# Kernel tuning notes

Hardware: AMD Instinct MI355X
Metric: run time of the kernel (lower is better)

## Reference

```python
import jax, jax.numpy as jnp
import numpy as np

EPS = 1e-8  # matches F.cosine_similarity default eps


def setup_inputs() -> dict:
    key = jax.random.key(0)
    k1, k2 = jax.random.split(key)
    labels = jax.random.uniform(k1, (8192, 2), dtype=jnp.float32)  # argmax -> random 0/1
    datas = jax.random.normal(k2, (8192, 4096), dtype=jnp.float32)
    return {"labels": labels, "datas": datas}


def reference(labels, datas):
    # labels: [B, C] one-hot (C=2); datas: [B, D]
    lab = jnp.argmax(labels, axis=1)
    mask0 = (lab == 0).astype(datas.dtype)  # normal vectors
    mask1 = (lab == 1).astype(datas.dtype)  # except vectors
    n0 = jnp.sum(mask0)
    n1 = jnp.sum(mask1)

    # mean of label-0 rows (fixed-shape masked mean instead of boolean gather)
    mean_vec = jnp.sum(datas * mask0[:, None], axis=0) / jnp.maximum(n0, 1.0)  # [D]

    # batched cosine similarity of every row vs mean_vec (replaces per-row loop)
    x_norm = jnp.maximum(jnp.linalg.norm(datas, axis=1), EPS)  # [B]
    m_norm = jnp.maximum(jnp.linalg.norm(mean_vec), EPS)       # scalar
    cos = (datas @ mean_vec) / (x_norm * m_norm)               # [B]
    abs_cos = jnp.abs(cos)

    sim_loss = jnp.sum(mask0 * (1.0 - abs_cos)) / jnp.maximum(n0, 1.0)
    differ_loss = jnp.sum(mask1 * abs_cos) / jnp.maximum(n1, 1.0)

    # edge cases: no normals -> both 0; normals but no excepts -> differ 0
    sim_loss = jnp.where(n0 > 0, sim_loss, 0.0)
    differ_loss = jnp.where((n0 > 0) & (n1 > 0), differ_loss, 0.0)
    total_loss = sim_loss + differ_loss
    return (total_loss, sim_loss, differ_loss)
```

## Files before the change

### kernel.cpp

```cpp
#include <hip/hip_runtime.h>
#include <math.h>

#define NROWS 8192
#define NCOLS 4096
#define NC4 1024
#define EPS 1e-8f

__device__ float g_partials[256 * NCOLS];
__device__ float g_S[NCOLS];
__device__ float g_n0[256];
__device__ float g_msq[256];
__device__ float g_A[1024];
__device__ float g_B[1024];

__global__ __launch_bounds__(256) void k_colsum(const float* __restrict__ labels,
                                                const float* __restrict__ datas) {
    const int b = blockIdx.x, t = threadIdx.x;
    const int rg = b >> 2, q = b & 3;
    const int r0 = rg * 32;
    __shared__ float m[32];
    __shared__ int idx[32];
    __shared__ int cntS;
    if (t < 32) {
        float l0 = labels[2 * (r0 + t)];
        float l1 = labels[2 * (r0 + t) + 1];
        m[t] = (l0 >= l1) ? 1.f : 0.f;
    }
    __syncthreads();
    if (t == 0) {
        int c = 0;
        #pragma unroll
        for (int r = 0; r < 32; ++r) if (m[r] != 0.f) idx[c++] = r0 + r;
        cntS = c;
        if (q == 0) g_n0[rg] = (float)c;
    }
    __syncthreads();
    const int cnt = cntS;
    const int coff = q * 256 + t;
    const float4* d4 = (const float4*)datas;
    float4 a0 = {0,0,0,0}, a1 = {0,0,0,0}, a2 = {0,0,0,0}, a3 = {0,0,0,0};
    int j = 0;
    for (; j + 3 < cnt; j += 4) {
        float4 v0 = d4[(size_t)idx[j]     * NC4 + coff];
        float4 v1 = d4[(size_t)idx[j + 1] * NC4 + coff];
        float4 v2 = d4[(size_t)idx[j + 2] * NC4 + coff];
        float4 v3 = d4[(size_t)idx[j + 3] * NC4 + coff];
        a0.x += v0.x; a0.y += v0.y; a0.z += v0.z; a0.w += v0.w;
        a1.x += v1.x; a1.y += v1.y; a1.z += v1.z; a1.w += v1.w;
        a2.x += v2.x; a2.y += v2.y; a2.z += v2.z; a2.w += v2.w;
        a3.x += v3.x; a3.y += v3.y; a3.z += v3.z; a3.w += v3.w;
    }
    for (; j < cnt; ++j) {
        float4 v = d4[(size_t)idx[j] * NC4 + coff];
        a0.x += v.x; a0.y += v.y; a0.z += v.z; a0.w += v.w;
    }
    a0.x += a1.x + a2.x + a3.x;
    a0.y += a1.y + a2.y + a3.y;
    a0.z += a1.z + a2.z + a3.z;
    a0.w += a1.w + a2.w + a3.w;
    ((float4*)g_partials)[(size_t)rg * NC4 + coff] = a0;
}

__global__ __launch_bounds__(256) void k_reduceS() {
    const int t = threadIdx.x, b = blockIdx.x;
    const int col = t & 15, sub = t >> 4;
    const int c = b * 16 + col;
    float s = 0.f;
    #pragma unroll
    for (int j = 0; j < 16; ++j)
        s += g_partials[(size_t)(sub * 16 + j) * NCOLS + c];
    __shared__ float sh[16][17];
    sh[sub][col] = s;
    __syncthreads();
    __shared__ float sh2[16];
    if (t < 16) {
        float tot = 0.f;
        #pragma unroll
        for (int i = 0; i < 16; ++i) tot += sh[i][t];
        g_S[c] = tot;
        sh2[t] = tot * tot;
    }
    __syncthreads();
    if (t == 0) {
        float sq = 0.f;
        #pragma unroll
        for (int i = 0; i < 16; ++i) sq += sh2[i];
        g_msq[b] = sq;
    }
}

__global__ __launch_bounds__(256) void k_cos(const float* __restrict__ labels,
                                             const float* __restrict__ datas) {
    const int t = threadIdx.x, lane = t & 63, w = t >> 6;
    const int rA = blockIdx.x * 8 + w * 2;
    const float4* d4 = (const float4*)datas;
    const float4* s4 = (const float4*)g_S;
    const size_t baseA = (size_t)rA * NC4;
    const size_t baseB = baseA + NC4;
    float dotA = 0.f, sqA = 0.f, dotB = 0.f, sqB = 0.f;
    float4 va[4], vb[4], sv[4];
    #pragma unroll
    for (int half = 0; half < 4; ++half) {
        const int k0 = half * 4;
        #pragma unroll
        for (int k = 0; k < 4; ++k) va[k] = d4[baseA + lane + ((k0 + k) << 6)];
        #pragma unroll
        for (int k = 0; k < 4; ++k) vb[k] = d4[baseB + lane + ((k0 + k) << 6)];
        #pragma unroll
        for (int k = 0; k < 4; ++k) sv[k] = s4[lane + ((k0 + k) << 6)];
        #pragma unroll
        for (int k = 0; k < 4; ++k) {
            dotA += va[k].x * sv[k].x + va[k].y * sv[k].y + va[k].z * sv[k].z + va[k].w * sv[k].w;
            sqA  += va[k].x * va[k].x + va[k].y * va[k].y + va[k].z * va[k].z + va[k].w * va[k].w;
            dotB += vb[k].x * sv[k].x + vb[k].y * sv[k].y + vb[k].z * sv[k].z + vb[k].w * sv[k].w;
            sqB  += vb[k].x * vb[k].x + vb[k].y * vb[k].y + vb[k].z * vb[k].z + vb[k].w * vb[k].w;
        }
    }
    #pragma unroll
    for (int off = 32; off; off >>= 1) {
        dotA += __shfl_xor(dotA, off);
        sqA  += __shfl_xor(sqA, off);
        dotB += __shfl_xor(dotB, off);
        sqB  += __shfl_xor(sqB, off);
    }
    __shared__ float shA[4], shB[4];
    if (lane == 0) {
        float aA = fabsf(dotA) / fmaxf(sqrtf(sqA), EPS);
        float aB = fabsf(dotB) / fmaxf(sqrtf(sqB), EPS);
        float lA0 = labels[2 * rA],     lA1 = labels[2 * rA + 1];
        float lB0 = labels[2 * rA + 2], lB1 = labels[2 * rA + 3];
        bool mA = (lA0 >= lA1), mB = (lB0 >= lB1);
        shA[w] = (mA ? aA : 0.f) + (mB ? aB : 0.f);
        shB[w] = (mA ? 0.f : aA) + (mB ? 0.f : aB);
    }
    __syncthreads();
    if (t == 0) {
        g_A[blockIdx.x] = shA[0] + shA[1] + shA[2] + shA[3];
        g_B[blockIdx.x] = shB[0] + shB[1] + shB[2] + shB[3];
    }
}

__global__ __launch_bounds__(1024) void k_final(float* __restrict__ out) {
    const int t = threadIdx.x, lane = t & 63, w = t >> 6;
    float A = g_A[t];
    float B = g_B[t];
    float n0 = (t < 256) ? g_n0[t] : 0.f;
    float msq = (t < 256) ? g_msq[t] : 0.f;
    #pragma unroll
    for (int off = 32; off; off >>= 1) {
        A   += __shfl_xor(A, off);
        B   += __shfl_xor(B, off);
        n0  += __shfl_xor(n0, off);
        msq += __shfl_xor(msq, off);
    }
    __shared__ float sh[16][4];
    if (lane == 0) { sh[w][0] = A; sh[w][1] = B; sh[w][2] = n0; sh[w][3] = msq; }
    __syncthreads();
    if (t == 0) {
        float At = 0.f, Bt = 0.f, n0t = 0.f, mt = 0.f;
        #pragma unroll
        for (int i = 0; i < 16; ++i) {
            At += sh[i][0]; Bt += sh[i][1]; n0t += sh[i][2]; mt += sh[i][3];
        }
        float n1 = (float)NROWS - n0t;
        float n0d = fmaxf(n0t, 1.f), n1d = fmaxf(n1, 1.f);
        float D = fmaxf(sqrtf(mt), n0d * EPS);
        float simL = (n0t > 0.f) ? (n0t - At / D) / n0d : 0.f;
        float difL = (n0t > 0.f && n1 > 0.f) ? (Bt / D) / n1d : 0.f;
        out[0] = simL + difL;
        out[1] = simL;
        out[2] = difL;
    }
}

extern "C" void kernel_launch(void* const* d_in, const int* in_sizes, int n_in,
                              void* d_out, int out_size, void* d_ws, size_t ws_size,
                              hipStream_t stream) {
    const float* labels = (const float*)d_in[0];
    const float* datas  = (const float*)d_in[1];
    float* out = (float*)d_out;

    k_colsum<<<1024, 256, 0, stream>>>(labels, datas);
    k_reduceS<<<256, 256, 0, stream>>>();
    k_cos<<<1024, 256, 0, stream>>>(labels, datas);
    k_final<<<1, 1024, 0, stream>>>(out);
}
```

Measured before the change: 208.0 us.

## Fold column reduction and final reduction into last-block epilogues via atomic counters

```diff
diff --git a/kernel.cpp b/kernel.cpp
--- a/kernel.cpp
+++ b/kernel.cpp
@@ -9,9 +9,11 @@
 __device__ float g_partials[256 * NCOLS];
 __device__ float g_S[NCOLS];
 __device__ float g_n0[256];
-__device__ float g_msq[256];
+__device__ float g_msq4[4];
 __device__ float g_A[1024];
 __device__ float g_B[1024];
+__device__ int   g_qcnt[4];
+__device__ int   g_cnt;
 
 __global__ __launch_bounds__(256) void k_colsum(const float* __restrict__ labels,
                                                 const float* __restrict__ datas) {
@@ -59,38 +61,38 @@
     a0.z += a1.z + a2.z + a3.z;
     a0.w += a1.w + a2.w + a3.w;
     ((float4*)g_partials)[(size_t)rg * NC4 + coff] = a0;
-}
 
-__global__ __launch_bounds__(256) void k_reduceS() {
-    const int t = threadIdx.x, b = blockIdx.x;
-    const int col = t & 15, sub = t >> 4;
-    const int c = b * 16 + col;
-    float s = 0.f;
-    #pragma unroll
-    for (int j = 0; j < 16; ++j)
-        s += g_partials[(size_t)(sub * 16 + j) * NCOLS + c];
-    __shared__ float sh[16][17];
-    sh[sub][col] = s;
+    __threadfence();
+    __shared__ int lastS;
+    if (t == 0) lastS = (atomicAdd(&g_qcnt[q], 1) == 255) ? 1 : 0;
     __syncthreads();
-    __shared__ float sh2[16];
-    if (t < 16) {
-        float tot = 0.f;
+    if (lastS) {
+        __threadfence();
+        const int col4 = q * 256 + t;
+        const float4* p4 = (const float4*)g_partials;
+        float4 s = {0,0,0,0};
+        #pragma unroll 16
+        for (int rgi = 0; rgi < 256; ++rgi) {
+            float4 v = p4[(size_t)rgi * NC4 + col4];
+            s.x += v.x; s.y += v.y; s.z += v.z; s.w += v.w;
+        }
+        ((float4*)g_S)[col4] = s;
+        float sq = s.x * s.x + s.y * s.y + s.z * s.z + s.w * s.w;
         #pragma unroll
-        for (int i = 0; i < 16; ++i) tot += sh[i][t];
-        g_S[c] = tot;
-        sh2[t] = tot * tot;
-    }
-    __syncthreads();
-    if (t == 0) {
-        float sq = 0.f;
-        #pragma unroll
-        for (int i = 0; i < 16; ++i) sq += sh2[i];
-        g_msq[b] = sq;
+        for (int off = 32; off; off >>= 1) sq += __shfl_xor(sq, off);
+        __shared__ float shq[4];
+        if ((t & 63) == 0) shq[t >> 6] = sq;
+        __syncthreads();
+        if (t == 0) {
+            g_msq4[q] = shq[0] + shq[1] + shq[2] + shq[3];
+            g_qcnt[q] = 0;
+        }
     }
 }
 
 __global__ __launch_bounds__(256) void k_cos(const float* __restrict__ labels,
-                                             const float* __restrict__ datas) {
+                                             const float* __restrict__ datas,
+                                             float* __restrict__ out) {
     const int t = threadIdx.x, lane = t & 63, w = t >> 6;
     const int rA = blockIdx.x * 8 + w * 2;
     const float4* d4 = (const float4*)datas;
@@ -138,38 +140,44 @@
         g_A[blockIdx.x] = shA[0] + shA[1] + shA[2] + shA[3];
         g_B[blockIdx.x] = shB[0] + shB[1] + shB[2] + shB[3];
     }
-}
 
-__global__ __launch_bounds__(1024) void k_final(float* __restrict__ out) {
-    const int t = threadIdx.x, lane = t & 63, w = t >> 6;
-    float A = g_A[t];
-    float B = g_B[t];
-    float n0 = (t < 256) ? g_n0[t] : 0.f;
-    float msq = (t < 256) ? g_msq[t] : 0.f;
-    #pragma unroll
-    for (int off = 32; off; off >>= 1) {
-        A   += __shfl_xor(A, off);
-        B   += __shfl_xor(B, off);
-        n0  += __shfl_xor(n0, off);
-        msq += __shfl_xor(msq, off);
-    }
-    __shared__ float sh[16][4];
-    if (lane == 0) { sh[w][0] = A; sh[w][1] = B; sh[w][2] = n0; sh[w][3] = msq; }
+    __threadfence();
+    __shared__ int lastS;
+    if (t == 0) lastS = (atomicAdd(&g_cnt, 1) == 1023) ? 1 : 0;
     __syncthreads();
-    if (t == 0) {
-        float At = 0.f, Bt = 0.f, n0t = 0.f, mt = 0.f;
+    if (lastS) {
+        __threadfence();
+        float A = 0.f, B = 0.f;
         #pragma unroll
-        for (int i = 0; i < 16; ++i) {
-            At += sh[i][0]; Bt += sh[i][1]; n0t += sh[i][2]; mt += sh[i][3];
+        for (int j = 0; j < 4; ++j) {
+            A += g_A[t + 256 * j];
+            B += g_B[t + 256 * j];
         }
-        float n1 = (float)NROWS - n0t;
-        float n0d = fmaxf(n0t, 1.f), n1d = fmaxf(n1, 1.f);
-        float D = fmaxf(sqrtf(mt), n0d * EPS);
-        float simL = (n0t > 0.f) ? (n0t - At / D) / n0d : 0.f;
-        float difL = (n0t > 0.f && n1 > 0.f) ? (Bt / D) / n1d : 0.f;
-        out[0] = simL + difL;
-        out[1] = simL;
-        out[2] = difL;
+        float n0 = g_n0[t];
+        #pragma unroll
+        for (int off = 32; off; off >>= 1) {
+            A  += __shfl_xor(A, off);
+            B  += __shfl_xor(B, off);
+            n0 += __shfl_xor(n0, off);
+        }
+        __shared__ float sh[4][3];
+        if (lane == 0) { sh[w][0] = A; sh[w][1] = B; sh[w][2] = n0; }
+        __syncthreads();
+        if (t == 0) {
+            float At = sh[0][0] + sh[1][0] + sh[2][0] + sh[3][0];
+            float Bt = sh[0][1] + sh[1][1] + sh[2][1] + sh[3][1];
+            float n0t = sh[0][2] + sh[1][2] + sh[2][2] + sh[3][2];
+            float mt = g_msq4[0] + g_msq4[1] + g_msq4[2] + g_msq4[3];
+            float n1 = (float)NROWS - n0t;
+            float n0d = fmaxf(n0t, 1.f), n1d = fmaxf(n1, 1.f);
+            float D = fmaxf(sqrtf(mt), n0d * EPS);
+            float simL = (n0t > 0.f) ? (n0t - At / D) / n0d : 0.f;
+            float difL = (n0t > 0.f && n1 > 0.f) ? (Bt / D) / n1d : 0.f;
+            out[0] = simL + difL;
+            out[1] = simL;
+            out[2] = difL;
+            g_cnt = 0;
+        }
     }
 }
 
@@ -181,7 +189,5 @@
     float* out = (float*)d_out;
 
     k_colsum<<<1024, 256, 0, stream>>>(labels, datas);
-    k_reduceS<<<256, 256, 0, stream>>>();
-    k_cos<<<1024, 256, 0, stream>>>(labels, datas);
-    k_final<<<1, 1024, 0, stream>>>(out);
+    k_cos<<<1024, 256, 0, stream>>>(labels, datas, out);
 }
```

Measured after the change: 583.3 us. +180.5%, slower.
